# Kernel optimization log

Hardware: AMD Instinct MI355X
Metric: run time of the kernel (lower is better)

## Reference

```python
import jax, jax.numpy as jnp
import numpy as np

DIM = 256

def setup_inputs() -> dict:
    key = jax.random.key(0)
    ks = jax.random.split(key, 7)
    B, S, D = 8, 4096, DIM
    scale = 1.0 / np.sqrt(D)
    x = jax.random.normal(ks[0], (B, S, D), dtype=jnp.float32)
    # torch Linear: y = x @ W.T + b, W is [out, in]
    Wq = jax.random.normal(ks[1], (D, D), dtype=jnp.float32) * scale
    Wk = jax.random.normal(ks[2], (D, D), dtype=jnp.float32) * scale
    Wv = jax.random.normal(ks[3], (D, D), dtype=jnp.float32) * scale
    bq = jax.random.normal(ks[4], (D,), dtype=jnp.float32) * 0.01
    bk = jax.random.normal(ks[5], (D,), dtype=jnp.float32) * 0.01
    bv = jax.random.normal(ks[6], (D,), dtype=jnp.float32) * 0.01
    return {"x": x, "Wq": Wq, "bq": bq, "Wk": Wk, "bk": bk, "Wv": Wv, "bv": bv}

def reference(x, Wq, bq, Wk, bk, Wv, bv):
    D = x.shape[-1]
    scale = D ** -0.5
    q = jnp.einsum('bsd,ed->bse', x, Wq) + bq  # [B,S,D]
    k = jnp.einsum('bsd,ed->bse', x, Wk) + bk
    v = jnp.einsum('bsd,ed->bse', x, Wv) + bv
    attn = jnp.einsum('bqd,bkd->bqk', q, k) * scale  # [B,S,S]
    attn = jax.nn.softmax(attn, axis=-1)
    return x + jnp.einsum('bqk,bkd->bqd', attn, v)
```

## Files before the change

### kernel.cpp

```cpp
#include <hip/hip_runtime.h>
#include <hip/hip_bf16.h>

typedef __attribute__((ext_vector_type(8))) short bf16x8;
typedef __attribute__((ext_vector_type(4))) float f32x4;
typedef __attribute__((ext_vector_type(16))) float f32x16;

#define MFMA16(a, b, c) __builtin_amdgcn_mfma_f32_16x16x32_bf16(a, b, c, 0, 0, 0)
#define MFMA32(a, b, c) __builtin_amdgcn_mfma_f32_32x32x16_bf16(a, b, c, 0, 0, 0)

__device__ __forceinline__ short f2bf(float f) {
    union { __hip_bfloat16 h; short s; } u;
    u.h = __float2bfloat16(f);
    return u.s;
}

__device__ __forceinline__ bf16x8 cvt8(const float* __restrict__ p) {
    f32x4 a = *reinterpret_cast<const f32x4*>(p);
    f32x4 b = *reinterpret_cast<const f32x4*>(p + 4);
    bf16x8 r;
    r[0] = f2bf(a[0]); r[1] = f2bf(a[1]); r[2] = f2bf(a[2]); r[3] = f2bf(a[3]);
    r[4] = f2bf(b[0]); r[5] = f2bf(b[1]); r[6] = f2bf(b[2]); r[7] = f2bf(b[3]);
    return r;
}

typedef __attribute__((address_space(1))) const unsigned int g_u32;
typedef __attribute__((address_space(3))) unsigned int l_u32;
__device__ __forceinline__ void gld16(const void* g, void* l) {
    __builtin_amdgcn_global_load_lds((g_u32*)(g), (l_u32*)(l), 16, 0, 0);
}

#define SBAR()    asm volatile("s_barrier" ::: "memory")
#define VMCNT(N)  asm volatile("s_waitcnt vmcnt(" #N ")" ::: "memory")

__global__ void wcvt_kernel(const float* __restrict__ Wq, const float* __restrict__ Wk,
                            const float* __restrict__ Wv, short* __restrict__ Wb)
{
    int t = blockIdx.x * 256 + threadIdx.x;
    int idx = t * 8;
    const float* src = idx < 65536 ? Wq + idx
                     : (idx < 131072 ? Wk + (idx - 65536) : Wv + (idx - 131072));
    *reinterpret_cast<bf16x8*>(Wb + idx) = cvt8(src);
}

__global__ __launch_bounds__(256, 2) void qkv_kernel(
    const float* __restrict__ x, const short* __restrict__ Wb,
    const float* __restrict__ bq, const float* __restrict__ bk, const float* __restrict__ bv,
    short* __restrict__ qo, short* __restrict__ ko, short* __restrict__ vto)
{
    const int wave = threadIdx.x >> 6, lane = threadIdx.x & 63;
    const int l31 = lane & 31, h = lane >> 5;
    const int row0 = blockIdx.x * 128;
    const int wrow = row0 + wave * 32;

    bf16x8 af[16];
    const float* __restrict__ xr = x + (size_t)(wrow + l31) * 256 + h * 8;
#pragma unroll
    for (int kc = 0; kc < 16; ++kc) af[kc] = cvt8(xr + kc * 16);

    __shared__ short tile[128][264];

    for (int proj = 0; proj < 3; ++proj) {
        const short* __restrict__ W = Wb + proj * 65536;
        const float* __restrict__ bias = proj == 0 ? bq : (proj == 1 ? bk : bv);

        f32x16 acc[8];
#pragma unroll
        for (int df = 0; df < 8; ++df)
#pragma unroll
            for (int e = 0; e < 16; ++e) acc[df][e] = 0.f;

#pragma unroll
        for (int kc = 0; kc < 16; ++kc)
#pragma unroll
            for (int df = 0; df < 8; ++df) {
                bf16x8 bfr = *reinterpret_cast<const bf16x8*>(
                    W + (df * 32 + l31) * 256 + kc * 16 + h * 8);
                acc[df] = MFMA32(af[kc], bfr, acc[df]);
            }

        if (proj < 2) {
            short* __restrict__ dst = proj == 0 ? qo : ko;
#pragma unroll
            for (int df = 0; df < 8; ++df) {
                int col = df * 32 + l31;
                float bv_ = bias[col];
#pragma unroll
                for (int rg = 0; rg < 16; ++rg) {
                    int r = (rg & 3) + 8 * (rg >> 2) + 4 * h;
                    dst[(size_t)(wrow + r) * 256 + col] = f2bf(acc[df][rg] + bv_);
                }
            }
        } else {
#pragma unroll
            for (int df = 0; df < 8; ++df) {
                int col = df * 32 + l31;
                float bv_ = bias[col];
#pragma unroll
                for (int rg = 0; rg < 16; ++rg) {
                    int r = (rg & 3) + 8 * (rg >> 2) + 4 * h;
                    tile[wave * 32 + r][col] = f2bf(acc[df][rg] + bv_);
                }
            }
            __syncthreads();
            int d = threadIdx.x;
            int bb = row0 >> 12, s0 = row0 & 4095;
            short* __restrict__ dst = vto + ((size_t)bb * 256 + d) * 4096 + s0;
#pragma unroll
            for (int i = 0; i < 16; ++i) {
                bf16x8 v;
#pragma unroll
                for (int j = 0; j < 8; ++j) v[j] = tile[i * 8 + j][d];
                *reinterpret_cast<bf16x8*>(dst + i * 8) = v;
            }
        }
    }
}

__global__ __launch_bounds__(256, 2) void attn_kernel(
    const short* __restrict__ q, const short* __restrict__ k,
    const short* __restrict__ vt, const float* __restrict__ x,
    float* __restrict__ out)
{
    const int id = blockIdx.x;
    const int b = id & 7, qt = id >> 3;
    const int tid = threadIdx.x;
    const int wave = tid >> 6, lane = tid & 63;
    const int l15 = lane & 15, l4 = lane >> 4;
    const int qrow0 = qt * 64 + wave * 16;

    const short* __restrict__ qb = q  + (size_t)b * 4096 * 256;
    const short* __restrict__ kb = k  + (size_t)b * 4096 * 256;
    const short* __restrict__ vb = vt + (size_t)b * 256 * 4096;

    __shared__ short smem[32768];
    __shared__ short plds[4][16][72];
    short (*pw)[72] = plds[wave];

    bf16x8 qf[8];
    const short* __restrict__ qr = qb + (size_t)(qrow0 + l15) * 256 + l4 * 8;
#pragma unroll
    for (int kc = 0; kc < 8; ++kc)
        qf[kc] = *reinterpret_cast<const bf16x8*>(qr + kc * 32);

    f32x4 o[16];
#pragma unroll
    for (int df = 0; df < 16; ++df) { f32x4 z = {0.f,0.f,0.f,0.f}; o[df] = z; }

    float ls[4] = {0.f, 0.f, 0.f, 0.f};
    const float cs = 0.0625f * 1.44269504f;

#define STAGE(T)                                                               \
  { _Pragma("unroll")                                                          \
    for (int i = 0; i < 16; ++i) {                                             \
        int c = i * 256 + tid;                                                 \
        int ss = c & 63;                                                       \
        const short* src;                                                      \
        if (c < 2048) {                                                        \
            int nf = c >> 9, kc = (c >> 6) & 7;                                \
            src = kb + (size_t)((T) * 64 + nf * 16 + (ss & 15)) * 256          \
                     + kc * 32 + (ss >> 4) * 8;                                \
        } else {                                                               \
            int df = (c >> 7) & 15, kc2 = (c >> 6) & 1;                        \
            src = vb + (size_t)(df * 16 + (ss & 15)) * 4096 + (T) * 64         \
                     + kc2 * 32 + (ss >> 4) * 8;                               \
        }                                                                      \
        gld16(src, &smem[c * 8]);                                              \
    } }

    STAGE(0);
    VMCNT(0);
    SBAR();
    __builtin_amdgcn_sched_barrier(0);

    const short* __restrict__ kb2 = smem;
    const short* __restrict__ vb2 = smem + 16384;

    for (int t = 0; t < 64; ++t) {
        f32x4 sacc[4];
#pragma unroll
        for (int nf = 0; nf < 4; ++nf) { f32x4 z = {0.f,0.f,0.f,0.f}; sacc[nf] = z; }
#pragma unroll
        for (int nf = 0; nf < 4; ++nf)
#pragma unroll
            for (int kc = 0; kc < 8; ++kc) {
                bf16x8 kf = *reinterpret_cast<const bf16x8*>(
                    kb2 + (nf * 512 + kc * 64 + lane) * 8);
                sacc[nf] = MFMA16(qf[kc], kf, sacc[nf]);
            }

#pragma unroll
        for (int nf = 0; nf < 4; ++nf)
#pragma unroll
            for (int r = 0; r < 4; ++r) {
                float p = exp2f(sacc[nf][r] * cs);
                ls[r] += p;
                pw[l4 * 4 + r][nf * 16 + l15] = f2bf(p);
            }
        bf16x8 pf0 = *reinterpret_cast<const bf16x8*>(&pw[l15][l4 * 8]);
        bf16x8 pf1 = *reinterpret_cast<const bf16x8*>(&pw[l15][32 + l4 * 8]);

#pragma unroll
        for (int df = 0; df < 16; ++df) {
            bf16x8 v0 = *reinterpret_cast<const bf16x8*>(
                vb2 + (df * 128 + lane) * 8);
            bf16x8 v1 = *reinterpret_cast<const bf16x8*>(
                vb2 + (df * 128 + 64 + lane) * 8);
            o[df] = MFMA16(pf0, v0, o[df]);
            o[df] = MFMA16(pf1, v1, o[df]);
        }

        SBAR();
        if (t < 63) {
            STAGE(t + 1);
            VMCNT(0);
        }
        SBAR();
        __builtin_amdgcn_sched_barrier(0);
    }

    float inv[4];
#pragma unroll
    for (int r = 0; r < 4; ++r) {
        float v = ls[r];
#pragma unroll
        for (int d = 1; d < 16; d <<= 1) v += __shfl_xor(v, d);
        inv[r] = 1.0f / v;
    }
#pragma unroll
    for (int r = 0; r < 4; ++r) {
        size_t row = (size_t)b * 4096 + qrow0 + l4 * 4 + r;
#pragma unroll
        for (int df = 0; df < 16; ++df) {
            int col = df * 16 + l15;
            out[row * 256 + col] = o[df][r] * inv[r] + x[row * 256 + col];
        }
    }
#undef STAGE
}

extern "C" void kernel_launch(void* const* d_in, const int* in_sizes, int n_in,
                              void* d_out, int out_size, void* d_ws, size_t ws_size,
                              hipStream_t stream) {
    const float* x  = (const float*)d_in[0];
    const float* Wq = (const float*)d_in[1];
    const float* bq = (const float*)d_in[2];
    const float* Wk = (const float*)d_in[3];
    const float* bk = (const float*)d_in[4];
    const float* Wv = (const float*)d_in[5];
    const float* bv = (const float*)d_in[6];
    float* out = (float*)d_out;

    char* ws = (char*)d_ws;
    short* qb  = (short*)ws;
    short* kb  = (short*)(ws + (size_t)16 * 1024 * 1024);
    short* vtb = (short*)(ws + (size_t)32 * 1024 * 1024);
    short* Wb  = (short*)d_out;

    wcvt_kernel<<<96, 256, 0, stream>>>(Wq, Wk, Wv, Wb);

    qkv_kernel<<<256, 256, 0, stream>>>(x, Wb, bq, bk, bv, qb, kb, vtb);

    attn_kernel<<<512, 256, 0, stream>>>(qb, kb, vtb, x, out);
}
```

Baseline: 328.7 us.

## Skew P·V by one tile and split K/V staging into separate phases

The K and V tile loads become separate staging macros. The P·V MFMA for tile t-1 now runs at the start of iteration t, before the QK^T MFMAs and the exp work for tile t, and a final P·V epilogue runs after the loop. The aim is to let the P·V matrix work and the score/softmax work interleave within one barrier region instead of being serialized. Global loads still wait on VMCNT(0) between barriers, so no load latency is actually hidden, and the extra epilogue adds code size.

```diff
diff --git a/kernel.cpp b/kernel.cpp
--- a/kernel.cpp
+++ b/kernel.cpp
@@ -149,25 +149,28 @@
     float ls[4] = {0.f, 0.f, 0.f, 0.f};
     const float cs = 0.0625f * 1.44269504f;
 
-#define STAGE(T)                                                               \
+#define STAGE_K(T)                                                             \
   { _Pragma("unroll")                                                          \
-    for (int i = 0; i < 16; ++i) {                                             \
+    for (int i = 0; i < 8; ++i) {                                              \
         int c = i * 256 + tid;                                                 \
         int ss = c & 63;                                                       \
-        const short* src;                                                      \
-        if (c < 2048) {                                                        \
-            int nf = c >> 9, kc = (c >> 6) & 7;                                \
-            src = kb + (size_t)((T) * 64 + nf * 16 + (ss & 15)) * 256          \
-                     + kc * 32 + (ss >> 4) * 8;                                \
-        } else {                                                               \
-            int df = (c >> 7) & 15, kc2 = (c >> 6) & 1;                        \
-            src = vb + (size_t)(df * 16 + (ss & 15)) * 4096 + (T) * 64         \
-                     + kc2 * 32 + (ss >> 4) * 8;                               \
-        }                                                                      \
-        gld16(src, &smem[c * 8]);                                              \
+        int nf = c >> 9, kc = (c >> 6) & 7;                                    \
+        gld16(kb + (size_t)((T) * 64 + nf * 16 + (ss & 15)) * 256              \
+                 + kc * 32 + (ss >> 4) * 8,                                    \
+              &smem[c * 8]);                                                   \
     } }
-
-    STAGE(0);
+#define STAGE_V(T)                                                             \
+  { _Pragma("unroll")                                                          \
+    for (int i = 0; i < 8; ++i) {                                              \
+        int c = i * 256 + tid;                                                 \
+        int ss = c & 63;                                                       \
+        int df = (c >> 7) & 15, kc2 = (c >> 6) & 1;                            \
+        gld16(vb + (size_t)(df * 16 + (ss & 15)) * 4096 + (T) * 64             \
+                 + kc2 * 32 + (ss >> 4) * 8,                                   \
+              &smem[(2048 + c) * 8]);                                          \
+    } }
+
+    STAGE_K(0);
     VMCNT(0);
     SBAR();
     __builtin_amdgcn_sched_barrier(0);
@@ -176,6 +179,20 @@
     const short* __restrict__ vb2 = smem + 16384;
 
     for (int t = 0; t < 64; ++t) {
+        if (t > 0) {
+            bf16x8 pf0 = *reinterpret_cast<const bf16x8*>(&pw[l15][l4 * 8]);
+            bf16x8 pf1 = *reinterpret_cast<const bf16x8*>(&pw[l15][32 + l4 * 8]);
+#pragma unroll
+            for (int df = 0; df < 16; ++df) {
+                bf16x8 v0 = *reinterpret_cast<const bf16x8*>(
+                    vb2 + (df * 128 + lane) * 8);
+                bf16x8 v1 = *reinterpret_cast<const bf16x8*>(
+                    vb2 + (df * 128 + 64 + lane) * 8);
+                o[df] = MFMA16(pf0, v0, o[df]);
+                o[df] = MFMA16(pf1, v1, o[df]);
+            }
+        }
+
         f32x4 sacc[4];
 #pragma unroll
         for (int nf = 0; nf < 4; ++nf) { f32x4 z = {0.f,0.f,0.f,0.f}; sacc[nf] = z; }
@@ -196,9 +213,18 @@
                 ls[r] += p;
                 pw[l4 * 4 + r][nf * 16 + l15] = f2bf(p);
             }
+
+        SBAR();
+        if (t < 63) STAGE_K(t + 1);
+        STAGE_V(t);
+        VMCNT(0);
+        SBAR();
+        __builtin_amdgcn_sched_barrier(0);
+    }
+
+    {
         bf16x8 pf0 = *reinterpret_cast<const bf16x8*>(&pw[l15][l4 * 8]);
         bf16x8 pf1 = *reinterpret_cast<const bf16x8*>(&pw[l15][32 + l4 * 8]);
-
 #pragma unroll
         for (int df = 0; df < 16; ++df) {
             bf16x8 v0 = *reinterpret_cast<const bf16x8*>(
@@ -208,14 +234,6 @@
             o[df] = MFMA16(pf0, v0, o[df]);
             o[df] = MFMA16(pf1, v1, o[df]);
         }
-
-        SBAR();
-        if (t < 63) {
-            STAGE(t + 1);
-            VMCNT(0);
-        }
-        SBAR();
-        __builtin_amdgcn_sched_barrier(0);
     }
 
     float inv[4];
@@ -235,7 +253,8 @@
             out[row * 256 + col] = o[df][r] * inv[r] + x[row * 256 + col];
         }
     }
-#undef STAGE
+#undef STAGE_K
+#undef STAGE_V
 }
 
 extern "C" void kernel_launch(void* const* d_in, const int* in_sizes, int n_in,
```

Result: slower. 344.0 us (+4.7%).

## Split each KV tile across two wave groups and reduce partial outputs in LDS

Applied to the files above, without the earlier changes.

Doubles the attention block to 8 waves. Each pair of waves shares 16 query rows and processes half of each 64-key tile (32 keys), then combines partial O accumulators and row sums through shared memory before the epilogue. This is meant to raise wave-level parallelism and latency hiding per block. In exchange it adds an LDS reduction step and tighter register limits from the higher launch bound, which may cause spills.

```diff
diff --git a/kernel.cpp b/kernel.cpp
--- a/kernel.cpp
+++ b/kernel.cpp
@@ -116,7 +116,7 @@
     }
 }
 
-__global__ __launch_bounds__(256, 2) void attn_kernel(
+__global__ __launch_bounds__(512, 4) void attn_kernel(
     const short* __restrict__ q, const short* __restrict__ k,
     const short* __restrict__ vt, const float* __restrict__ x,
     float* __restrict__ out)
@@ -126,15 +126,16 @@
     const int tid = threadIdx.x;
     const int wave = tid >> 6, lane = tid & 63;
     const int l15 = lane & 15, l4 = lane >> 4;
-    const int qrow0 = qt * 64 + wave * 16;
+    const int qg = wave & 3, hh = wave >> 2;
+    const int qrow0 = qt * 64 + qg * 16;
 
     const short* __restrict__ qb = q  + (size_t)b * 4096 * 256;
     const short* __restrict__ kb = k  + (size_t)b * 4096 * 256;
     const short* __restrict__ vb = vt + (size_t)b * 256 * 4096;
 
     __shared__ short smem[32768];
-    __shared__ short plds[4][16][72];
-    short (*pw)[72] = plds[wave];
+    __shared__ short plds[8][16][40];
+    short (*pw)[40] = plds[wave];
 
     bf16x8 qf[8];
     const short* __restrict__ qr = qb + (size_t)(qrow0 + l15) * 256 + l4 * 8;
@@ -151,18 +152,18 @@
 
 #define STAGE(T)                                                               \
   { _Pragma("unroll")                                                          \
-    for (int i = 0; i < 16; ++i) {                                             \
-        int c = i * 256 + tid;                                                 \
-        int ss = c & 63;                                                       \
+    for (int i = 0; i < 8; ++i) {                                              \
+        int c = i * 512 + tid;                                                 \
         const short* src;                                                      \
         if (c < 2048) {                                                        \
-            int nf = c >> 9, kc = (c >> 6) & 7;                                \
-            src = kb + (size_t)((T) * 64 + nf * 16 + (ss & 15)) * 256          \
-                     + kc * 32 + (ss >> 4) * 8;                                \
+            int hh_ = c >> 10, nf = (c >> 9) & 1, kc = (c >> 6) & 7, l = c & 63;\
+            src = kb + (size_t)((T) * 64 + hh_ * 32 + nf * 16 + (l & 15)) * 256\
+                     + kc * 32 + (l >> 4) * 8;                                 \
         } else {                                                               \
-            int df = (c >> 7) & 15, kc2 = (c >> 6) & 1;                        \
-            src = vb + (size_t)(df * 16 + (ss & 15)) * 4096 + (T) * 64         \
-                     + kc2 * 32 + (ss >> 4) * 8;                               \
+            int s = c & 2047;                                                  \
+            int hh_ = s >> 10, df = (s >> 6) & 15, l = s & 63;                 \
+            src = vb + (size_t)(df * 16 + (l & 15)) * 4096 + (T) * 64          \
+                     + hh_ * 32 + (l >> 4) * 8;                                \
         }                                                                      \
         gld16(src, &smem[c * 8]);                                              \
     } }
@@ -172,41 +173,37 @@
     SBAR();
     __builtin_amdgcn_sched_barrier(0);
 
-    const short* __restrict__ kb2 = smem;
-    const short* __restrict__ vb2 = smem + 16384;
+    const short* __restrict__ kbase = smem + hh * 1024 * 8;
+    const short* __restrict__ vbase = smem + (2048 + hh * 1024) * 8;
 
     for (int t = 0; t < 64; ++t) {
-        f32x4 sacc[4];
-#pragma unroll
-        for (int nf = 0; nf < 4; ++nf) { f32x4 z = {0.f,0.f,0.f,0.f}; sacc[nf] = z; }
-#pragma unroll
-        for (int nf = 0; nf < 4; ++nf)
+        f32x4 sacc[2];
+#pragma unroll
+        for (int nf = 0; nf < 2; ++nf) { f32x4 z = {0.f,0.f,0.f,0.f}; sacc[nf] = z; }
+#pragma unroll
+        for (int nf = 0; nf < 2; ++nf)
 #pragma unroll
             for (int kc = 0; kc < 8; ++kc) {
                 bf16x8 kf = *reinterpret_cast<const bf16x8*>(
-                    kb2 + (nf * 512 + kc * 64 + lane) * 8);
+                    kbase + (nf * 512 + kc * 64 + lane) * 8);
                 sacc[nf] = MFMA16(qf[kc], kf, sacc[nf]);
             }
 
 #pragma unroll
-        for (int nf = 0; nf < 4; ++nf)
+        for (int nf = 0; nf < 2; ++nf)
 #pragma unroll
             for (int r = 0; r < 4; ++r) {
                 float p = exp2f(sacc[nf][r] * cs);
                 ls[r] += p;
                 pw[l4 * 4 + r][nf * 16 + l15] = f2bf(p);
             }
-        bf16x8 pf0 = *reinterpret_cast<const bf16x8*>(&pw[l15][l4 * 8]);
-        bf16x8 pf1 = *reinterpret_cast<const bf16x8*>(&pw[l15][32 + l4 * 8]);
+        bf16x8 pf = *reinterpret_cast<const bf16x8*>(&pw[l15][l4 * 8]);
 
 #pragma unroll
         for (int df = 0; df < 16; ++df) {
-            bf16x8 v0 = *reinterpret_cast<const bf16x8*>(
-                vb2 + (df * 128 + lane) * 8);
-            bf16x8 v1 = *reinterpret_cast<const bf16x8*>(
-                vb2 + (df * 128 + 64 + lane) * 8);
-            o[df] = MFMA16(pf0, v0, o[df]);
-            o[df] = MFMA16(pf1, v1, o[df]);
+            bf16x8 vf = *reinterpret_cast<const bf16x8*>(
+                vbase + (df * 64 + lane) * 8);
+            o[df] = MFMA16(pf, vf, o[df]);
         }
 
         SBAR();
@@ -218,21 +215,43 @@
         __builtin_amdgcn_sched_barrier(0);
     }
 
-    float inv[4];
 #pragma unroll
     for (int r = 0; r < 4; ++r) {
         float v = ls[r];
 #pragma unroll
         for (int d = 1; d < 16; d <<= 1) v += __shfl_xor(v, d);
-        inv[r] = 1.0f / v;
-    }
-#pragma unroll
-    for (int r = 0; r < 4; ++r) {
-        size_t row = (size_t)b * 4096 + qrow0 + l4 * 4 + r;
+        ls[r] = v;
+    }
+
+    f32x4* __restrict__ fo = (f32x4*)smem;
+    float* __restrict__ fl = (float*)plds;
+
+    __syncthreads();
+
+    if (hh == 1) {
+#pragma unroll
+        for (int df = 0; df < 16; ++df)
+            fo[(qg * 16 + df) * 64 + lane] = o[df];
+#pragma unroll
+        for (int r = 0; r < 4; ++r)
+            fl[(qg * 4 + r) * 64 + lane] = ls[r];
+    }
+    __syncthreads();
+
+    if (hh == 0) {
+        float inv[4];
+#pragma unroll
+        for (int r = 0; r < 4; ++r)
+            inv[r] = 1.0f / (ls[r] + fl[(qg * 4 + r) * 64 + lane]);
 #pragma unroll
         for (int df = 0; df < 16; ++df) {
+            f32x4 od = fo[(qg * 16 + df) * 64 + lane];
             int col = df * 16 + l15;
-            out[row * 256 + col] = o[df][r] * inv[r] + x[row * 256 + col];
+#pragma unroll
+            for (int r = 0; r < 4; ++r) {
+                size_t row = (size_t)b * 4096 + qrow0 + l4 * 4 + r;
+                out[row * 256 + col] = (o[df][r] + od[r]) * inv[r] + x[row * 256 + col];
+            }
         }
     }
 #undef STAGE
@@ -260,5 +279,5 @@
 
     qkv_kernel<<<256, 256, 0, stream>>>(x, Wb, bq, bk, bv, qb, kb, vtb);
 
-    attn_kernel<<<512, 256, 0, stream>>>(qb, kb, vtb, x, out);
-}
+    attn_kernel<<<512, 512, 0, stream>>>(qb, kb, vtb, x, out);
+}
```

Measured after the change: 713.2 us. 117% more time.
